# Optimization experiments

Hardware: AMD Instinct MI355X
Metric: run time of the kernel (lower is better)

The kernel has to match this reference:

```python
import jax, jax.numpy as jnp
import numpy as np

NU = 100000
NV = 100000
EF = 500000
EB = 500000
D = 64  # e_in = u_in = v_in = e_out = 64; u_out = v_out = 64 -> nu_dim = nv_dim = 32
DC = D + D  # concat dim: node_in + e_in = 128


def _lin(key, din, dout):
    kw, kb = jax.random.split(key)
    lim = 1.0 / np.sqrt(din)
    W = jax.random.uniform(kw, (din, dout), jnp.float32, -lim, lim)
    b = jax.random.uniform(kb, (dout,), jnp.float32, -lim, lim)
    return W, b


def setup_inputs() -> dict:
    key = jax.random.key(0)
    ks = jax.random.split(key, 20)
    inp = {
        'f_feat': jax.random.normal(ks[0], (EF, D), jnp.float32),
        'b_feat': jax.random.normal(ks[1], (EB, D), jnp.float32),
        'u_feat': jax.random.normal(ks[2], (NU, D), jnp.float32),
        'v_feat': jax.random.normal(ks[3], (NV, D), jnp.float32),
        'fsrc': jax.random.randint(ks[4], (EF,), 0, NU, jnp.int32),
        'fdst': jax.random.randint(ks[5], (EF,), 0, NV, jnp.int32),
        'bsrc': jax.random.randint(ks[6], (EB,), 0, NV, jnp.int32),
        'bdst': jax.random.randint(ks[7], (EB,), 0, NU, jnp.int32),
    }
    inp['We'], inp['be'] = _lin(ks[8], D, D)        # e_linear
    inp['Wul'], inp['bul'] = _lin(ks[9], D, D)      # u_linear
    inp['Wvl'], inp['bvl'] = _lin(ks[10], D, D)     # v_linear
    inp['Wau'], inp['bau'] = _lin(ks[11], D, DC)    # W_ATTN_u: u_in -> v_in+e_in
    inp['Wav'], inp['bav'] = _lin(ks[12], D, DC)    # W_ATTN_v: v_in -> u_in+e_in
    inp['Wwu'], inp['bwu'] = _lin(ks[13], DC, D // 2)  # W_u
    inp['Wwv'], inp['bwv'] = _lin(ks[14], DC, D // 2)  # W_v
    inp['WVu'], inp['bVu'] = _lin(ks[15], D, D - D // 2)  # Vu
    inp['WVv'], inp['bVv'] = _lin(ks[16], D, D - D // 2)  # Vv
    return inp


def _edge_softmax(scores, dst, n):
    # scores: [E,1]; softmax over edges grouped by destination node
    m = jax.ops.segment_max(scores, dst, num_segments=n)
    e = jnp.exp(scores - m[dst])
    s = jax.ops.segment_sum(e, dst, num_segments=n)
    return e / s[dst]


def reference(f_feat, b_feat, u_feat, v_feat, fsrc, fdst, bsrc, bdst,
              We, be, Wul, bul, Wvl, bvl, Wau, bau, Wav, bav,
              Wwu, bwu, Wwv, bwv, WVu, bVu, WVv, bVv):
    Nu, Nv = u_feat.shape[0], v_feat.shape[0]
    he_u = u_feat @ Wul + bul
    he_v = v_feat @ Wvl + bvl
    # edge hidden: he_e + he of incident u and v (activation is None, dropout 0)
    hf = f_feat @ We + be + he_u[fsrc] + he_v[fdst]   # forward: src=u, dst=v
    hb = b_feat @ We + be + he_v[bsrc] + he_u[bdst]   # backward: src=v, dst=u
    # concat raw src node feat with raw edge feat
    h_ue = jnp.concatenate([u_feat[fsrc], f_feat], axis=-1)  # [EF, DC]
    h_ve = jnp.concatenate([v_feat[bsrc], b_feat], axis=-1)  # [EB, DC]
    att_u = u_feat @ Wau + bau  # [Nu, DC]
    att_v = v_feat @ Wav + bav  # [Nv, DC]
    s_f = jnp.sum(h_ue * att_v[fdst], axis=-1, keepdims=True)  # e_dot_v
    s_b = jnp.sum(h_ve * att_u[bdst], axis=-1, keepdims=True)
    sfm_f = _edge_softmax(s_f, fdst, Nv)
    sfm_b = _edge_softmax(s_b, bdst, Nu)
    agg_v = jax.ops.segment_sum(h_ue * sfm_f, fdst, num_segments=Nv)
    agg_u = jax.ops.segment_sum(h_ve * sfm_b, bdst, num_segments=Nu)
    h_nu = agg_u @ Wwu + bwu
    h_nv = agg_v @ Wwv + bwv
    hu = jnp.concatenate([u_feat @ WVu + bVu, h_nu], axis=-1)
    hv = jnp.concatenate([v_feat @ WVv + bVv, h_nv], axis=-1)
    return hf, hb, hu, hv
```

## Files before the change

kernel.cpp:

```cpp
#include <hip/hip_runtime.h>
#include <hip/hip_bf16.h>
#include <cstdint>

typedef __attribute__((ext_vector_type(4))) float f32x4;
typedef __attribute__((ext_vector_type(8))) short bf16x8;
typedef __attribute__((ext_vector_type(4))) unsigned short u16x4;

__device__ inline unsigned short f2bf(float f) {
    union { float f; unsigned u; } v; v.f = f;
    unsigned r = v.u + 0x7FFFu + ((v.u >> 16) & 1u);
    return (unsigned short)(r >> 16);
}
__device__ inline float bf2f(unsigned short h) {
    union { unsigned u; float f; } v; v.u = ((unsigned)h) << 16;
    return v.f;
}

__global__ void prep_kernel(
    const float* __restrict__ We,
    const float* __restrict__ Wul, const float* __restrict__ Wau, const float* __restrict__ WVu,
    const float* __restrict__ Wvl, const float* __restrict__ Wav, const float* __restrict__ WVv,
    const float* __restrict__ Wwu, const float* __restrict__ Wwv,
    const float* __restrict__ bul, const float* __restrict__ bau, const float* __restrict__ bVu,
    const float* __restrict__ bvl, const float* __restrict__ bav, const float* __restrict__ bVv,
    unsigned short* __restrict__ WeXf, unsigned short* __restrict__ WeXb,
    unsigned short* __restrict__ WnTu, unsigned short* __restrict__ WnTv,
    float* __restrict__ bcu, float* __restrict__ bcv)
{
    int tid0 = blockIdx.x * blockDim.x + threadIdx.x;
    int stride = gridDim.x * blockDim.x;
    for (int i = tid0; i < 176 * 64; i += stride) {
        int c = i >> 6, k = i & 63;
        float vf, vb;
        if (c < 64)       { vf = We[k * 64 + c];               vb = vf; }
        else if (c < 96)  { vf = Wwv[(64 + k) * 32 + (c - 64)]; vb = Wwu[(64 + k) * 32 + (c - 64)]; }
        else if (c < 160) { vf = Wav[(c - 96) * 128 + 64 + k];  vb = Wau[(c - 96) * 128 + 64 + k]; }
        else if (c == 160){ vf = bav[64 + k];                   vb = bau[64 + k]; }
        else              { vf = 0.f;                           vb = 0.f; }
        WeXf[i] = f2bf(vf);
        WeXb[i] = f2bf(vb);
    }
    for (int i = tid0; i < 272 * 64; i += stride) {
        int c = i >> 6, k = i & 63;
        float vu, vv;
        if (c < 64)       { vu = Wul[k * 64 + c];           vv = Wvl[k * 64 + c]; }
        else if (c < 128) { vu = Wav[(c - 64) * 128 + k];   vv = Wau[(c - 64) * 128 + k]; }
        else if (c < 160) { vu = WVu[k * 32 + (c - 128)];   vv = WVv[k * 32 + (c - 128)]; }
        else if (c < 192) { vu = Wwv[k * 32 + (c - 160)];   vv = Wwu[k * 32 + (c - 160)]; }
        else if (c == 192){ vu = bav[k];                    vv = bau[k]; }
        else if (c < 208) { vu = 0.f;                       vv = 0.f; }
        else              { vu = (k == c - 208) ? 1.f : 0.f; vv = vu; }
        WnTu[i] = f2bf(vu);
        WnTv[i] = f2bf(vv);
    }
    for (int i = tid0; i < 208; i += stride) {
        float u = 0.f, v = 0.f;
        if (i < 64)                { u = bul[i];       v = bvl[i]; }
        else if (i >= 128 && i < 160) { u = bVu[i - 128]; v = bVv[i - 128]; }
        bcu[i] = u; bcv[i] = v;
    }
}

__global__ __launch_bounds__(256, 4) void node_pre_kernel(
    int nbU, int NU, int NV,
    const float* __restrict__ featU, const float* __restrict__ featV,
    const unsigned short* __restrict__ WTu, const unsigned short* __restrict__ WTv,
    const float* __restrict__ bcu, const float* __restrict__ bcv,
    unsigned short* __restrict__ heU, unsigned short* __restrict__ heV,
    unsigned short* __restrict__ ztU, unsigned short* __restrict__ ztV,
    unsigned short* __restrict__ nbfU, unsigned short* __restrict__ nbfV,
    float* __restrict__ outU, float* __restrict__ outV,
    unsigned short* __restrict__ projU, unsigned short* __restrict__ projV,
    float* __restrict__ sbU, float* __restrict__ sbV,
    float* __restrict__ aggU, float* __restrict__ aggV,
    float* __restrict__ wsU, float* __restrict__ wsV)
{
    bool isu = (int)blockIdx.x < nbU;
    int blk = isu ? blockIdx.x : blockIdx.x - nbU;
    int N = isu ? NU : NV;
    const float* feat = isu ? featU : featV;
    const unsigned short* WT = isu ? WTu : WTv;
    const float* bc = isu ? bcu : bcv;
    unsigned short* he = isu ? heU : heV;
    unsigned short* zt = isu ? ztU : ztV;
    unsigned short* nbf = isu ? nbfU : nbfV;
    float* outp = isu ? outU : outV;
    unsigned short* proj = isu ? projU : projV;
    float* sb = isu ? sbU : sbV;
    float* agg32 = isu ? aggU : aggV;
    float* ws = isu ? wsU : wsV;

    __shared__ unsigned short lW[272 * 64];
    int tid = threadIdx.x;
    int n0 = blk * 64;

    const uint4* wsrc = (const uint4*)WT;
    for (int i = tid; i < 272 * 8; i += 256) {
        int r = i >> 3, ch = i & 7;
        *(uint4*)&lW[r * 64 + ((ch ^ (r & 7)) << 3)] = wsrc[i];
    }
    {
        for (int i = tid; i < 64 * 32; i += 256) {
            int n = n0 + (i >> 5);
            if (n < N) agg32[(size_t)n * 32 + (i & 31)] = 0.f;
        }
        if (tid < 64) { int n = n0 + tid; if (n < N) ws[n] = 0.f; }
    }

    int wv = tid >> 6, lane = tid & 63;
    int r0 = wv * 16;
    int lrow = lane & 15, lkg = lane >> 4;

    int nr = n0 + r0 + lrow;
    bool rok = nr < N;
    const float* arow = &feat[(size_t)nr * 64];
    bf16x8 a[2];
    #pragma unroll
    for (int h = 0; h < 2; ++h) {
        int ch = h * 4 + lkg;
        f32x4 v0 = (f32x4){0.f, 0.f, 0.f, 0.f}, v1 = v0;
        if (rok) {
            v0 = __builtin_nontemporal_load((const f32x4*)&arow[ch * 8]);
            v1 = __builtin_nontemporal_load((const f32x4*)&arow[ch * 8 + 4]);
        }
        bf16x8 av;
        av[0] = (short)f2bf(v0.x); av[1] = (short)f2bf(v0.y);
        av[2] = (short)f2bf(v0.z); av[3] = (short)f2bf(v0.w);
        av[4] = (short)f2bf(v1.x); av[5] = (short)f2bf(v1.y);
        av[6] = (short)f2bf(v1.z); av[7] = (short)f2bf(v1.w);
        a[h] = av;
    }
    __syncthreads();

    f32x4 acc[17];
    #pragma unroll
    for (int t = 0; t < 17; ++t) acc[t] = (f32x4){0.f, 0.f, 0.f, 0.f};
    #pragma unroll
    for (int t = 0; t < 17; ++t) {
        int row = t * 16 + lrow;
        #pragma unroll
        for (int h = 0; h < 2; ++h) {
            int ch = h * 4 + lkg;
            bf16x8 b = *(const bf16x8*)&lW[row * 64 + ((ch ^ (row & 7)) << 3)];
            acc[t] = __builtin_amdgcn_mfma_f32_16x16x32_bf16(a[h], b, acc[t], 0, 0, 0);
        }
    }
    #pragma unroll
    for (int t = 0; t < 17; ++t) {
        #pragma unroll
        for (int q = 0; q < 4; ++q) {
            int n = n0 + r0 + lkg * 4 + q;
            if (n >= N) continue;
            int c = t * 16 + lrow;
            float raw = acc[t][q];
            if (t < 4) {
                he[(size_t)n * 64 + lrow * 4 + t] = f2bf(raw + bc[c]);
            } else if (t < 8) {
                zt[(size_t)n * 64 + lrow * 4 + (t - 4)] = f2bf(raw);
            } else if (t < 10) {
                __builtin_nontemporal_store(raw + bc[c], &outp[(size_t)n * 64 + (c - 128)]);
            } else if (t < 12) {
                proj[(size_t)n * 32 + (c - 160)] = f2bf(raw);
            } else if (t == 12) {
                if (lrow == 0) sb[n] = raw;
            } else {
                nbf[(size_t)n * 64 + lrow * 4 + (t - 13)] = f2bf(raw);
            }
        }
    }
}

__global__ __launch_bounds__(256, 5) void edge_kernel(
    int nbF, int EF, int EB,
    const float* __restrict__ efF, const float* __restrict__ efB,
    const int* __restrict__ srcF, const int* __restrict__ dstF,
    const int* __restrict__ srcB, const int* __restrict__ dstB,
    const unsigned short* __restrict__ zF, const unsigned short* __restrict__ zB,
    const float* __restrict__ sbF, const float* __restrict__ sbB,
    const unsigned short* __restrict__ projF, const unsigned short* __restrict__ projB,
    const unsigned short* __restrict__ heSF, const unsigned short* __restrict__ heSB,
    const unsigned short* __restrict__ heDF, const unsigned short* __restrict__ heDB,
    const unsigned short* __restrict__ nbfF, const unsigned short* __restrict__ nbfB,
    const unsigned short* __restrict__ WeXF, const unsigned short* __restrict__ WeXB,
    const float* __restrict__ be,
    float* __restrict__ outF, float* __restrict__ outB,
    float* __restrict__ aggF, float* __restrict__ aggB,
    float* __restrict__ wsF, float* __restrict__ wsB)
{
    bool fwd = (int)blockIdx.x < nbF;
    int blk = fwd ? blockIdx.x : blockIdx.x - nbF;
    int E = fwd ? EF : EB;
    const float* efeat = fwd ? efF : efB;
    const int* src = fwd ? srcF : srcB;
    const int* dst = fwd ? dstF : dstB;
    const unsigned short* z_src = fwd ? zF : zB;
    const float* sb_src = fwd ? sbF : sbB;
    const unsigned short* proj_src = fwd ? projF : projB;
    const unsigned short* he_src = fwd ? heSF : heSB;
    const unsigned short* he_dst = fwd ? heDF : heDB;
    const unsigned short* nbf_dst = fwd ? nbfF : nbfB;
    const unsigned short* WeX = fwd ? WeXF : WeXB;
    float* out_he = fwd ? outF : outB;
    float* agg32 = fwd ? aggF : aggB;
    float* wsum = fwd ? wsF : wsB;

    __shared__ unsigned short lW[176 * 64];
    int tid = threadIdx.x;
    int lane = tid & 63;
    int wvu = __builtin_amdgcn_readfirstlane(tid >> 6);
    int e0 = blk * 64;
    int eBase = e0 + wvu * 16;
    int lrow = lane & 15, lkg = lane >> 4;

    const uint4* wsrc = (const uint4*)WeX;
    for (int i = tid; i < 176 * 8; i += 256) {
        int r = i >> 3, ch = i & 7;
        *(uint4*)&lW[r * 64 + ((ch ^ (r & 7)) << 3)] = wsrc[i];
    }

    int sil[4], dil[4];
    #pragma unroll
    for (int j = 0; j < 4; ++j) {
        int e = eBase + lkg * 4 + j;
        sil[j] = (e < E) ? src[e] : 0;
        dil[j] = (e < E) ? dst[e] : 0;
    }

    int er = eBase + lrow;
    bool rok = er < E;
    const float* arow = &efeat[(size_t)er * 64];
    bf16x8 a[2];
    #pragma unroll
    for (int h = 0; h < 2; ++h) {
        int ch = h * 4 + lkg;
        f32x4 v0 = (f32x4){0.f, 0.f, 0.f, 0.f}, v1 = v0;
        if (rok) {
            v0 = __builtin_nontemporal_load((const f32x4*)&arow[ch * 8]);
            v1 = __builtin_nontemporal_load((const f32x4*)&arow[ch * 8 + 4]);
        }
        bf16x8 av;
        av[0] = (short)f2bf(v0.x); av[1] = (short)f2bf(v0.y);
        av[2] = (short)f2bf(v0.z); av[3] = (short)f2bf(v0.w);
        av[4] = (short)f2bf(v1.x); av[5] = (short)f2bf(v1.y);
        av[6] = (short)f2bf(v1.z); av[7] = (short)f2bf(v1.w);
        a[h] = av;
    }
    __syncthreads();

    f32x4 acc[11];
    #pragma unroll
    for (int t = 0; t < 11; ++t) acc[t] = (f32x4){0.f, 0.f, 0.f, 0.f};
    #pragma unroll
    for (int t = 0; t < 11; ++t) {
        int row = t * 16 + lrow;
        #pragma unroll
        for (int h = 0; h < 2; ++h) {
            int ch = h * 4 + lkg;
            bf16x8 b = *(const bf16x8*)&lW[row * 64 + ((ch ^ (row & 7)) << 3)];
            acc[t] = __builtin_amdgcn_mfma_f32_16x16x32_bf16(a[h], b, acc[t], 0, 0, 0);
        }
    }

    float wq[4];
    #pragma unroll
    for (int j = 0; j < 4; ++j) {
        int e = eBase + lkg * 4 + j;
        float p = acc[10][j];
        if (e < E) {
            int si = sil[j], di = dil[j];
            u16x4 zr = *(const u16x4*)&z_src[(size_t)si * 64 + lrow * 4];
            u16x4 vr = *(const u16x4*)&nbf_dst[(size_t)di * 64 + lrow * 4];
            #pragma unroll
            for (int tt = 0; tt < 4; ++tt) {
                float zv = bf2f(zr[tt]) + acc[6 + tt][j];
                p += zv * bf2f(vr[tt]);
            }
            if (lrow == 1) p += sb_src[si];
        }
        p += __shfl_xor(p, 1, 64);
        p += __shfl_xor(p, 2, 64);
        p += __shfl_xor(p, 4, 64);
        p += __shfl_xor(p, 8, 64);
        wq[j] = __expf(p);
    }

    #pragma unroll
    for (int j = 0; j < 4; ++j) {
        int e = eBase + lkg * 4 + j;
        if (e >= E) continue;
        float w = wq[j];
        int si = sil[j], di = dil[j];
        #pragma unroll
        for (int h = 0; h < 2; ++h) {
            int c = lrow + h * 16;
            float pv = bf2f(proj_src[(size_t)si * 32 + c]) + acc[4 + h][j];
            unsafeAtomicAdd(&agg32[(size_t)di * 32 + c], w * pv);
        }
        if (lrow == 2) unsafeAtomicAdd(&wsum[di], w);
    }

    float bev[4];
    #pragma unroll
    for (int t = 0; t < 4; ++t) bev[t] = be[t * 16 + lrow];
    #pragma unroll
    for (int q = 0; q < 4; ++q) {
        int e = eBase + lkg * 4 + q;
        if (e >= E) continue;
        int si = sil[q], di = dil[q];
        u16x4 hs4 = *(const u16x4*)&he_src[(size_t)si * 64 + lrow * 4];
        u16x4 hd4 = *(const u16x4*)&he_dst[(size_t)di * 64 + lrow * 4];
        #pragma unroll
        for (int t = 0; t < 4; ++t) {
            int c = t * 16 + lrow;
            __builtin_nontemporal_store(acc[t][q] + bev[t] + bf2f(hs4[t]) + bf2f(hd4[t]),
                                        &out_he[(size_t)e * 64 + c]);
        }
    }
}

__global__ void finalize_kernel(const float* __restrict__ aggU, const float* __restrict__ wsU,
                                const float* __restrict__ aggV, const float* __restrict__ wsV,
                                int NU, int NV,
                                const float* __restrict__ bwu, const float* __restrict__ bwv,
                                float* __restrict__ outU, float* __restrict__ outV)
{
    int idx = blockIdx.x * blockDim.x + threadIdx.x;
    int tot = (NU + NV) * 32;
    if (idx >= tot) return;
    bool isu = idx < NU * 32;
    int li = isu ? idx : idx - NU * 32;
    int n = li >> 5, c = li & 31;
    const float* agg = isu ? aggU : aggV;
    const float* ws = isu ? wsU : wsV;
    const float* bias = isu ? bwu : bwv;
    float* outp = isu ? outU : outV;
    float s = ws[n];
    float sc = (s > 0.f) ? 1.0f / s : 0.f;
    __builtin_nontemporal_store(agg[li] * sc + bias[c], &outp[(size_t)n * 64 + 32 + c]);
}

extern "C" void kernel_launch(void* const* d_in, const int* in_sizes, int n_in,
                              void* d_out, int out_size, void* d_ws, size_t ws_size,
                              hipStream_t stream)
{
    const float* f_feat = (const float*)d_in[0];
    const float* b_feat = (const float*)d_in[1];
    const float* u_feat = (const float*)d_in[2];
    const float* v_feat = (const float*)d_in[3];
    const int* fsrc = (const int*)d_in[4];
    const int* fdst = (const int*)d_in[5];
    const int* bsrc = (const int*)d_in[6];
    const int* bdst = (const int*)d_in[7];
    const float* We  = (const float*)d_in[8];
    const float* be  = (const float*)d_in[9];
    const float* Wul = (const float*)d_in[10];
    const float* bul = (const float*)d_in[11];
    const float* Wvl = (const float*)d_in[12];
    const float* bvl = (const float*)d_in[13];
    const float* Wau = (const float*)d_in[14];
    const float* bau = (const float*)d_in[15];
    const float* Wav = (const float*)d_in[16];
    const float* bav = (const float*)d_in[17];
    const float* Wwu = (const float*)d_in[18];
    const float* bwu = (const float*)d_in[19];
    const float* Wwv = (const float*)d_in[20];
    const float* bwv = (const float*)d_in[21];
    const float* WVu = (const float*)d_in[22];
    const float* bVu = (const float*)d_in[23];
    const float* WVv = (const float*)d_in[24];
    const float* bVv = (const float*)d_in[25];

    int EF = in_sizes[0] / 64;
    int EB = in_sizes[1] / 64;
    int NU = in_sizes[2] / 64;
    int NV = in_sizes[3] / 64;

    float* out = (float*)d_out;
    float* hf = out;
    float* hb = hf + (size_t)EF * 64;
    float* hu = hb + (size_t)EB * 64;
    float* hv = hu + (size_t)NU * 64;

    char* wp = (char*)d_ws;
    auto alloc = [&](size_t bytes) { char* p = wp; wp += (bytes + 255) & ~(size_t)255; return p; };
    unsigned short* he_u  = (unsigned short*)alloc((size_t)NU * 64 * 2);
    unsigned short* he_v  = (unsigned short*)alloc((size_t)NV * 64 * 2);
    unsigned short* z_u   = (unsigned short*)alloc((size_t)NU * 64 * 2);
    unsigned short* z_v   = (unsigned short*)alloc((size_t)NV * 64 * 2);
    unsigned short* nbf_u = (unsigned short*)alloc((size_t)NU * 64 * 2);
    unsigned short* nbf_v = (unsigned short*)alloc((size_t)NV * 64 * 2);
    unsigned short* proj_u = (unsigned short*)alloc((size_t)NU * 32 * 2);
    unsigned short* proj_v = (unsigned short*)alloc((size_t)NV * 32 * 2);
    float* sb_u   = (float*)alloc((size_t)NU * 4);
    float* sb_v   = (float*)alloc((size_t)NV * 4);
    float* agg_u  = (float*)alloc((size_t)NU * 32 * 4);
    float* agg_v  = (float*)alloc((size_t)NV * 32 * 4);
    float* ws_u   = (float*)alloc((size_t)NU * 4);
    float* ws_v   = (float*)alloc((size_t)NV * 4);
    unsigned short* WeXf = (unsigned short*)alloc(176 * 64 * 2);
    unsigned short* WeXb = (unsigned short*)alloc(176 * 64 * 2);
    unsigned short* WnTu = (unsigned short*)alloc(272 * 64 * 2);
    unsigned short* WnTv = (unsigned short*)alloc(272 * 64 * 2);
    float* bcu = (float*)alloc(208 * 4);
    float* bcv = (float*)alloc(208 * 4);

    prep_kernel<<<64, 256, 0, stream>>>(We, Wul, Wau, WVu, Wvl, Wav, WVv, Wwu, Wwv,
                                        bul, bau, bVu, bvl, bav, bVv,
                                        WeXf, WeXb, WnTu, WnTv, bcu, bcv);

    int nbU = (NU + 63) / 64, nbV = (NV + 63) / 64;
    node_pre_kernel<<<nbU + nbV, 256, 0, stream>>>(nbU, NU, NV, u_feat, v_feat,
                                                   WnTu, WnTv, bcu, bcv,
                                                   he_u, he_v, z_u, z_v, nbf_u, nbf_v,
                                                   hu, hv, proj_u, proj_v, sb_u, sb_v,
                                                   agg_u, agg_v, ws_u, ws_v);

    int nbF = (EF + 63) / 64, nbB = (EB + 63) / 64;
    edge_kernel<<<nbF + nbB, 256, 0, stream>>>(nbF, EF, EB, f_feat, b_feat,
                                               fsrc, fdst, bsrc, bdst,
                                               z_u, z_v, sb_u, sb_v, proj_u, proj_v,
                                               he_u, he_v, he_v, he_u,
                                               nbf_v, nbf_u,
                                               WeXf, WeXb, be,
                                               hf, hb, agg_v, agg_u, ws_v, ws_u);

    finalize_kernel<<<((NU + NV) * 32 + 255) / 256, 256, 0, stream>>>(
        agg_u, ws_u, agg_v, ws_v, NU, NV, bwu, bwv, hu, hv);
}
```

Baseline: 349.7 us.

## Interleave per-node gather tables so each edge fetches one 16-byte row per endpoint

The node pre-pass now writes two interleaved tables per node type, srcT holding z and he, and dstT holding the neighbour projection and he, so that each lane reads one 16-byte vector per endpoint instead of separate 8-byte gathers from three arrays. The edge-feature output store is moved ahead of the atomic aggregation and reuses the already gathered values, removing the second round of he gathers. The cost is that he is written twice (duplicated into both tables) in the node pass. Gathers are now issued even for out-of-range edges, which relies on the index buffers holding safe values there.

```diff
diff --git a/kernel.cpp b/kernel.cpp
--- a/kernel.cpp
+++ b/kernel.cpp
@@ -4,7 +4,7 @@
 
 typedef __attribute__((ext_vector_type(4))) float f32x4;
 typedef __attribute__((ext_vector_type(8))) short bf16x8;
-typedef __attribute__((ext_vector_type(4))) unsigned short u16x4;
+typedef __attribute__((ext_vector_type(8))) unsigned short u16x8;
 
 __device__ inline unsigned short f2bf(float f) {
     union { float f; unsigned u; } v; v.f = f;
@@ -66,9 +66,8 @@
     const float* __restrict__ featU, const float* __restrict__ featV,
     const unsigned short* __restrict__ WTu, const unsigned short* __restrict__ WTv,
     const float* __restrict__ bcu, const float* __restrict__ bcv,
-    unsigned short* __restrict__ heU, unsigned short* __restrict__ heV,
-    unsigned short* __restrict__ ztU, unsigned short* __restrict__ ztV,
-    unsigned short* __restrict__ nbfU, unsigned short* __restrict__ nbfV,
+    unsigned short* __restrict__ srcTU, unsigned short* __restrict__ srcTV,
+    unsigned short* __restrict__ dstTU, unsigned short* __restrict__ dstTV,
     float* __restrict__ outU, float* __restrict__ outV,
     unsigned short* __restrict__ projU, unsigned short* __restrict__ projV,
     float* __restrict__ sbU, float* __restrict__ sbV,
@@ -81,9 +80,8 @@
     const float* feat = isu ? featU : featV;
     const unsigned short* WT = isu ? WTu : WTv;
     const float* bc = isu ? bcu : bcv;
-    unsigned short* he = isu ? heU : heV;
-    unsigned short* zt = isu ? ztU : ztV;
-    unsigned short* nbf = isu ? nbfU : nbfV;
+    unsigned short* srcT = isu ? srcTU : srcTV;
+    unsigned short* dstT = isu ? dstTU : dstTV;
     float* outp = isu ? outU : outV;
     unsigned short* proj = isu ? projU : projV;
     float* sb = isu ? sbU : sbV;
@@ -154,9 +152,11 @@
             int c = t * 16 + lrow;
             float raw = acc[t][q];
             if (t < 4) {
-                he[(size_t)n * 64 + lrow * 4 + t] = f2bf(raw + bc[c]);
+                unsigned short hv = f2bf(raw + bc[c]);
+                srcT[(size_t)n * 128 + lrow * 8 + 4 + t] = hv;
+                dstT[(size_t)n * 128 + lrow * 8 + 4 + t] = hv;
             } else if (t < 8) {
-                zt[(size_t)n * 64 + lrow * 4 + (t - 4)] = f2bf(raw);
+                srcT[(size_t)n * 128 + lrow * 8 + (t - 4)] = f2bf(raw);
             } else if (t < 10) {
                 __builtin_nontemporal_store(raw + bc[c], &outp[(size_t)n * 64 + (c - 128)]);
             } else if (t < 12) {
@@ -164,7 +164,7 @@
             } else if (t == 12) {
                 if (lrow == 0) sb[n] = raw;
             } else {
-                nbf[(size_t)n * 64 + lrow * 4 + (t - 13)] = f2bf(raw);
+                dstT[(size_t)n * 128 + lrow * 8 + (t - 13)] = f2bf(raw);
             }
         }
     }
@@ -175,12 +175,10 @@
     const float* __restrict__ efF, const float* __restrict__ efB,
     const int* __restrict__ srcF, const int* __restrict__ dstF,
     const int* __restrict__ srcB, const int* __restrict__ dstB,
-    const unsigned short* __restrict__ zF, const unsigned short* __restrict__ zB,
+    const unsigned short* __restrict__ srcTU, const unsigned short* __restrict__ srcTV,
+    const unsigned short* __restrict__ dstTU, const unsigned short* __restrict__ dstTV,
     const float* __restrict__ sbF, const float* __restrict__ sbB,
     const unsigned short* __restrict__ projF, const unsigned short* __restrict__ projB,
-    const unsigned short* __restrict__ heSF, const unsigned short* __restrict__ heSB,
-    const unsigned short* __restrict__ heDF, const unsigned short* __restrict__ heDB,
-    const unsigned short* __restrict__ nbfF, const unsigned short* __restrict__ nbfB,
     const unsigned short* __restrict__ WeXF, const unsigned short* __restrict__ WeXB,
     const float* __restrict__ be,
     float* __restrict__ outF, float* __restrict__ outB,
@@ -193,12 +191,10 @@
     const float* efeat = fwd ? efF : efB;
     const int* src = fwd ? srcF : srcB;
     const int* dst = fwd ? dstF : dstB;
-    const unsigned short* z_src = fwd ? zF : zB;
+    const unsigned short* srcT = fwd ? srcTU : srcTV;
+    const unsigned short* dstT = fwd ? dstTV : dstTU;
     const float* sb_src = fwd ? sbF : sbB;
     const unsigned short* proj_src = fwd ? projF : projB;
-    const unsigned short* he_src = fwd ? heSF : heSB;
-    const unsigned short* he_dst = fwd ? heDF : heDB;
-    const unsigned short* nbf_dst = fwd ? nbfF : nbfB;
     const unsigned short* WeX = fwd ? WeXF : WeXB;
     float* out_he = fwd ? outF : outB;
     float* agg32 = fwd ? aggF : aggB;
@@ -261,19 +257,20 @@
         }
     }
 
+    u16x8 sr_[4], dr_[4];
     float wq[4];
     #pragma unroll
     for (int j = 0; j < 4; ++j) {
         int e = eBase + lkg * 4 + j;
+        int si = sil[j], di = dil[j];
+        sr_[j] = *(const u16x8*)&srcT[(size_t)si * 128 + lrow * 8];
+        dr_[j] = *(const u16x8*)&dstT[(size_t)di * 128 + lrow * 8];
         float p = acc[10][j];
         if (e < E) {
-            int si = sil[j], di = dil[j];
-            u16x4 zr = *(const u16x4*)&z_src[(size_t)si * 64 + lrow * 4];
-            u16x4 vr = *(const u16x4*)&nbf_dst[(size_t)di * 64 + lrow * 4];
             #pragma unroll
             for (int tt = 0; tt < 4; ++tt) {
-                float zv = bf2f(zr[tt]) + acc[6 + tt][j];
-                p += zv * bf2f(vr[tt]);
+                float zv = bf2f(sr_[j][tt]) + acc[6 + tt][j];
+                p += zv * bf2f(dr_[j][tt]);
             }
             if (lrow == 1) p += sb_src[si];
         }
@@ -282,6 +279,22 @@
         p += __shfl_xor(p, 4, 64);
         p += __shfl_xor(p, 8, 64);
         wq[j] = __expf(p);
+    }
+
+    float bev[4];
+    #pragma unroll
+    for (int t = 0; t < 4; ++t) bev[t] = be[t * 16 + lrow];
+    #pragma unroll
+    for (int q = 0; q < 4; ++q) {
+        int e = eBase + lkg * 4 + q;
+        if (e >= E) continue;
+        #pragma unroll
+        for (int t = 0; t < 4; ++t) {
+            int c = t * 16 + lrow;
+            __builtin_nontemporal_store(
+                acc[t][q] + bev[t] + bf2f(sr_[q][4 + t]) + bf2f(dr_[q][4 + t]),
+                &out_he[(size_t)e * 64 + c]);
+        }
     }
 
     #pragma unroll
@@ -297,24 +310,6 @@
             unsafeAtomicAdd(&agg32[(size_t)di * 32 + c], w * pv);
         }
         if (lrow == 2) unsafeAtomicAdd(&wsum[di], w);
-    }
-
-    float bev[4];
-    #pragma unroll
-    for (int t = 0; t < 4; ++t) bev[t] = be[t * 16 + lrow];
-    #pragma unroll
-    for (int q = 0; q < 4; ++q) {
-        int e = eBase + lkg * 4 + q;
-        if (e >= E) continue;
-        int si = sil[q], di = dil[q];
-        u16x4 hs4 = *(const u16x4*)&he_src[(size_t)si * 64 + lrow * 4];
-        u16x4 hd4 = *(const u16x4*)&he_dst[(size_t)di * 64 + lrow * 4];
-        #pragma unroll
-        for (int t = 0; t < 4; ++t) {
-            int c = t * 16 + lrow;
-            __builtin_nontemporal_store(acc[t][q] + bev[t] + bf2f(hs4[t]) + bf2f(hd4[t]),
-                                        &out_he[(size_t)e * 64 + c]);
-        }
     }
 }
 
@@ -383,12 +378,10 @@
 
     char* wp = (char*)d_ws;
     auto alloc = [&](size_t bytes) { char* p = wp; wp += (bytes + 255) & ~(size_t)255; return p; };
-    unsigned short* he_u  = (unsigned short*)alloc((size_t)NU * 64 * 2);
-    unsigned short* he_v  = (unsigned short*)alloc((size_t)NV * 64 * 2);
-    unsigned short* z_u   = (unsigned short*)alloc((size_t)NU * 64 * 2);
-    unsigned short* z_v   = (unsigned short*)alloc((size_t)NV * 64 * 2);
-    unsigned short* nbf_u = (unsigned short*)alloc((size_t)NU * 64 * 2);
-    unsigned short* nbf_v = (unsigned short*)alloc((size_t)NV * 64 * 2);
+    unsigned short* srcT_u = (unsigned short*)alloc((size_t)NU * 128 * 2);
+    unsigned short* srcT_v = (unsigned short*)alloc((size_t)NV * 128 * 2);
+    unsigned short* dstT_u = (unsigned short*)alloc((size_t)NU * 128 * 2);
+    unsigned short* dstT_v = (unsigned short*)alloc((size_t)NV * 128 * 2);
     unsigned short* proj_u = (unsigned short*)alloc((size_t)NU * 32 * 2);
     unsigned short* proj_v = (unsigned short*)alloc((size_t)NV * 32 * 2);
     float* sb_u   = (float*)alloc((size_t)NU * 4);
@@ -411,16 +404,15 @@
     int nbU = (NU + 63) / 64, nbV = (NV + 63) / 64;
     node_pre_kernel<<<nbU + nbV, 256, 0, stream>>>(nbU, NU, NV, u_feat, v_feat,
                                                    WnTu, WnTv, bcu, bcv,
-                                                   he_u, he_v, z_u, z_v, nbf_u, nbf_v,
+                                                   srcT_u, srcT_v, dstT_u, dstT_v,
                                                    hu, hv, proj_u, proj_v, sb_u, sb_v,
                                                    agg_u, agg_v, ws_u, ws_v);
 
     int nbF = (EF + 63) / 64, nbB = (EB + 63) / 64;
     edge_kernel<<<nbF + nbB, 256, 0, stream>>>(nbF, EF, EB, f_feat, b_feat,
                                                fsrc, fdst, bsrc, bdst,
-                                               z_u, z_v, sb_u, sb_v, proj_u, proj_v,
-                                               he_u, he_v, he_v, he_u,
-                                               nbf_v, nbf_u,
+                                               srcT_u, srcT_v, dstT_u, dstT_v,
+                                               sb_u, sb_v, proj_u, proj_v,
                                                WeXf, WeXb, be,
                                                hf, hb, agg_v, agg_u, ws_v, ws_u);
 
```

Measured after the change: 455.0 us. +30.1%, slower.
